# Kernel tuning notes

Measured on AMD Instinct MI355X. Metric: run time of the kernel, lower is better.

Reference implementation:

```python
import jax, jax.numpy as jnp
import numpy as np

TEMP = 5.0      # torch_kmeans SoftKMeans default temperature
N_ITERS = 25    # fixed iteration count (tolerance-based stop removed for jit)
EPS = 1e-9


def _soft_kmeans(x, l, key):
    # x: (r, q, d) -> labels (r, q) int32, centers (r, l, d)
    r, q, d = x.shape
    keys = jax.random.split(key, r)
    # random-point init (one permutation per batch, first l points)
    idx = jax.vmap(lambda k: jax.random.permutation(k, q)[:l])(keys)  # (r, l)
    centers = jnp.take_along_axis(x, idx[:, :, None], axis=1)         # (r, l, d)
    x_sq = jnp.sum(x * x, axis=-1)                                    # (r, q)

    def dist_to(centers):
        # squared euclidean distance (r, q, l)
        return (x_sq[:, :, None]
                - 2.0 * jnp.einsum('rqd,rld->rql', x, centers)
                + jnp.sum(centers * centers, axis=-1)[:, None, :])

    def step(centers, _):
        w = jax.nn.softmax(-TEMP * dist_to(centers), axis=-1)         # (r, q, l)
        denom = jnp.sum(w, axis=1)[:, :, None] + EPS                  # (r, l, 1)
        centers = jnp.einsum('rql,rqd->rld', w, x) / denom
        return centers, None

    centers, _ = jax.lax.scan(step, centers, None, length=N_ITERS)
    labels = jnp.argmin(dist_to(centers), axis=-1)                    # (r, q)
    return labels, centers


def setup_inputs() -> dict:
    key = jax.random.key(0)
    x = jax.random.normal(key, (8, 2048, 1024), dtype=jnp.float32)
    return {"x": x, "q": 4096, "r": 8, "l": 256}


def reference(x, q, r, l):
    B, T, F = x.shape
    # B*T*F must equal r*q*d; mirrors x.view(B,-1).view(B,q,-1).view(r,q,-1)
    xr = x.reshape(r, q, -1)
    labels, centers = _soft_kmeans(xr, l, jax.random.key(42))
    # gather centroid per point: rec[b, i, :] = centers[b, labels[b, i], :]
    rec = jnp.take_along_axis(centers, labels[:, :, None], axis=1)    # (r, q, d)
    return rec.reshape(B, T, F)
```

## Files before the change

### kernel.cpp

```cpp
#include <hip/hip_runtime.h>
#include <stdint.h>

#define RB 8
#define QN 4096
#define DN 512
#define LN 256
#define NITERS 25

__device__ __forceinline__ void tf2x32(uint32_t k0, uint32_t k1,
                                       uint32_t x0, uint32_t x1,
                                       uint32_t& y0, uint32_t& y1) {
  uint32_t ks2 = k0 ^ k1 ^ 0x1BD11BDAu;
#define TFR(r) { x0 += x1; x1 = (x1 << (r)) | (x1 >> (32 - (r))); x1 ^= x0; }
  x0 += k0; x1 += k1;
  TFR(13) TFR(15) TFR(26) TFR(6)   x0 += k1;  x1 += ks2 + 1u;
  TFR(17) TFR(29) TFR(16) TFR(24)  x0 += ks2; x1 += k0 + 2u;
  TFR(13) TFR(15) TFR(26) TFR(6)   x0 += k0;  x1 += k1 + 3u;
  TFR(17) TFR(29) TFR(16) TFR(24)  x0 += k1;  x1 += ks2 + 4u;
  TFR(13) TFR(15) TFR(26) TFR(6)   x0 += ks2; x1 += k0 + 5u;
#undef TFR
  y0 = x0; y1 = x1;
}

__global__ __launch_bounds__(1024) void k_init(const float* __restrict__ x,
                                               float* __restrict__ centers) {
  __shared__ unsigned long long comp[QN];
  __shared__ unsigned short perm[QN];
  __shared__ unsigned short ptmp[QN];
  const int b = blockIdx.x, t = threadIdx.x;

  uint32_t kb0, kb1;
  tf2x32(0u, 42u, 0u, (uint32_t)b, kb0, kb1);

  for (int i = t; i < QN; i += 1024) perm[i] = (unsigned short)i;
  __syncthreads();

  for (int round = 0; round < 2; ++round) {
    uint32_t nk0, nk1, sk0, sk1;
    tf2x32(kb0, kb1, 0u, 0u, nk0, nk1);
    tf2x32(kb0, kb1, 0u, 1u, sk0, sk1);
    kb0 = nk0; kb1 = nk1;
    for (int i = t; i < QN; i += 1024) {
      uint32_t y0, y1;
      tf2x32(sk0, sk1, 0u, (uint32_t)i, y0, y1);
      uint32_t bits = y0 ^ y1;
      comp[i] = ((unsigned long long)bits << 32) | (unsigned)i;
    }
    __syncthreads();
    for (int k = 2; k <= QN; k <<= 1) {
      for (int j = k >> 1; j > 0; j >>= 1) {
        for (int i = t; i < QN; i += 1024) {
          int ixj = i ^ j;
          if (ixj > i) {
            unsigned long long vi = comp[i], vj = comp[ixj];
            bool up = ((i & k) == 0);
            bool sw = up ? (vi > vj) : (vi < vj);
            if (sw) { comp[i] = vj; comp[ixj] = vi; }
          }
        }
        __syncthreads();
      }
    }
    for (int i = t; i < QN; i += 1024) ptmp[i] = perm[(unsigned)(comp[i] & 0xFFFFu)];
    __syncthreads();
    for (int i = t; i < QN; i += 1024) perm[i] = ptmp[i];
    __syncthreads();
  }

  const float4* xb = (const float4*)(x + (size_t)b * QN * DN);
  float4* cb = (float4*)(centers + (size_t)b * LN * DN);
  for (int e = t; e < LN * (DN / 4); e += 1024) {
    int row = e >> 7;
    int c = e & 127;
    cb[(size_t)row * 128 + c] = xb[(size_t)perm[row] * 128 + c];
  }
}

__global__ __launch_bounds__(256) void k_rowsq_d(const float* __restrict__ a,
                                                 double* __restrict__ o, int nrows) {
  int w = (blockIdx.x * 256 + threadIdx.x) >> 6;
  int lane = threadIdx.x & 63;
  if (w >= nrows) return;
  const float* row = a + (size_t)w * DN;
  double s = 0.0;
  for (int i = lane; i < DN; i += 64) { double v = (double)row[i]; s = fma(v, v, s); }
#pragma unroll
  for (int off = 32; off; off >>= 1) s += __shfl_down(s, off);
  if (lane == 0) o[w] = s;
}

#define QT 64
#define DK 16
#define XLD 82
#define CLDf 260
__device__ __forceinline__ int grow(int q) { return q + ((q >> 3) << 1); }

__global__ __launch_bounds__(256, 2) void k_assign(const float* __restrict__ x,
                                                   const float* __restrict__ centers,
                                                   const double* __restrict__ csqd,
                                                   float* __restrict__ W) {
  __shared__ double xsD[DK][XLD];
  __shared__ float  csF[DK][CLDf];
  __shared__ double red[QT][33];
  const int b = blockIdx.y, q0 = blockIdx.x * QT, t = threadIdx.x;
  const int rg = t & 7, cg = t >> 3;
  double acc[8][8];
#pragma unroll
  for (int i = 0; i < 8; i++)
#pragma unroll
    for (int j = 0; j < 8; j++) acc[i][j] = 0.0;

  const float* xb = x + ((size_t)b * QN + q0) * DN;
  const float* cb = centers + (size_t)b * LN * DN;
  const int xrow = t >> 2, xc4 = t & 3;
  const int xg = grow(xrow);

  float4 gx, gc[4];
  gx = *(const float4*)(xb + (size_t)xrow * DN + xc4 * 4);
#pragma unroll
  for (int i = 0; i < 4; i++) {
    int f = t + 256 * i; int row = f >> 2, c4 = f & 3;
    gc[i] = *(const float4*)(cb + (size_t)row * DN + c4 * 4);
  }

  for (int d0 = 0; d0 < DN; d0 += DK) {
    xsD[xc4 * 4 + 0][xg] = (double)gx.x; xsD[xc4 * 4 + 1][xg] = (double)gx.y;
    xsD[xc4 * 4 + 2][xg] = (double)gx.z; xsD[xc4 * 4 + 3][xg] = (double)gx.w;
#pragma unroll
    for (int i = 0; i < 4; i++) {
      int f = t + 256 * i; int row = f >> 2, c4 = f & 3;
      csF[c4 * 4 + 0][row] = gc[i].x; csF[c4 * 4 + 1][row] = gc[i].y;
      csF[c4 * 4 + 2][row] = gc[i].z; csF[c4 * 4 + 3][row] = gc[i].w;
    }
    __syncthreads();
    if (d0 + DK < DN) {
      gx = *(const float4*)(xb + (size_t)xrow * DN + (d0 + DK) + xc4 * 4);
#pragma unroll
      for (int i = 0; i < 4; i++) {
        int f = t + 256 * i; int row = f >> 2, c4 = f & 3;
        gc[i] = *(const float4*)(cb + (size_t)row * DN + (d0 + DK) + c4 * 4);
      }
    }
    double xva[8]; float4 ca0, ca1;
#pragma unroll
    for (int j = 0; j < 8; j++) xva[j] = xsD[0][rg * 10 + j];
    ca0 = *(const float4*)&csF[0][cg * 8];
    ca1 = *(const float4*)&csF[0][cg * 8 + 4];
#pragma unroll
    for (int k = 0; k < DK; k++) {
      double xvb[8]; float4 cb0, cb1;
      if (k + 1 < DK) {
#pragma unroll
        for (int j = 0; j < 8; j++) xvb[j] = xsD[k + 1][rg * 10 + j];
        cb0 = *(const float4*)&csF[k + 1][cg * 8];
        cb1 = *(const float4*)&csF[k + 1][cg * 8 + 4];
      }
      double cv[8] = {(double)ca0.x, (double)ca0.y, (double)ca0.z, (double)ca0.w,
                      (double)ca1.x, (double)ca1.y, (double)ca1.z, (double)ca1.w};
#pragma unroll
      for (int i = 0; i < 8; i++)
#pragma unroll
        for (int j = 0; j < 8; j++)
          acc[i][j] = fma(xva[i], cv[j], acc[i][j]);
      if (k + 1 < DK) {
#pragma unroll
        for (int j = 0; j < 8; j++) xva[j] = xvb[j];
        ca0 = cb0; ca1 = cb1;
      }
    }
    __syncthreads();
  }

  double csqv[8];
#pragma unroll
  for (int j = 0; j < 8; j++) csqv[j] = csqd[b * LN + cg * 8 + j];

  double lmax[8];
#pragma unroll
  for (int i = 0; i < 8; i++) {
    double m = -1e300;
#pragma unroll
    for (int j = 0; j < 8; j++) {
      double lg = -5.0 * (csqv[j] - 2.0 * acc[i][j]);
      acc[i][j] = lg;
      m = fmax(m, lg);
    }
    lmax[i] = m;
  }
#pragma unroll
  for (int i = 0; i < 8; i++) red[rg * 8 + i][cg] = lmax[i];
  __syncthreads();
  double rmax[8];
#pragma unroll
  for (int i = 0; i < 8; i++) {
    double m = -1e300;
    for (int c = 0; c < 32; c++) m = fmax(m, red[rg * 8 + i][c]);
    rmax[i] = m;
  }
  __syncthreads();
#pragma unroll
  for (int i = 0; i < 8; i++) {
    double s = 0.0;
#pragma unroll
    for (int j = 0; j < 8; j++) {
      double e = exp(acc[i][j] - rmax[i]);
      acc[i][j] = e;
      s += e;
    }
    red[rg * 8 + i][cg] = s;
  }
  __syncthreads();
#pragma unroll
  for (int i = 0; i < 8; i++) {
    double s = 0.0;
    for (int c = 0; c < 32; c++) s += red[rg * 8 + i][c];
    float* wrow = W + ((size_t)b * QN + q0 + rg * 8 + i) * LN + cg * 8;
    float4 v0 = make_float4((float)(acc[i][0] / s), (float)(acc[i][1] / s),
                            (float)(acc[i][2] / s), (float)(acc[i][3] / s));
    float4 v1 = make_float4((float)(acc[i][4] / s), (float)(acc[i][5] / s),
                            (float)(acc[i][6] / s), (float)(acc[i][7] / s));
    *(float4*)wrow = v0;
    *(float4*)(wrow + 4) = v1;
  }
}

#define NCH 8
#define CHQ (QN / NCH)
#define UKQ 16

__global__ __launch_bounds__(256, 2) void k_update_split(
    const float* __restrict__ W, const float* __restrict__ x,
    float* __restrict__ P, float* __restrict__ dsum) {
  __shared__ float wT[UKQ][132];
  __shared__ float xT[UKQ][132];
  const int b = blockIdx.z;
  const int s = blockIdx.y;
  const int lt = (blockIdx.x >> 2) * 128;
  const int dt = (blockIdx.x & 3) * 128;
  const int t = threadIdx.x;
  const int tr = t >> 4, tc = t & 15;
  float acc[8][8];
#pragma unroll
  for (int i = 0; i < 8; i++)
#pragma unroll
    for (int j = 0; j < 8; j++) acc[i][j] = 0.f;
  float dsm[8] = {0, 0, 0, 0, 0, 0, 0, 0};

  const float* Wb = W + ((size_t)b * QN + (size_t)s * CHQ) * LN + lt;
  const float* xb = x + ((size_t)b * QN + (size_t)s * CHQ) * DN + dt;

  float4 gw[2], gx2[2];
#pragma unroll
  for (int i = 0; i < 2; i++) {
    int f = t + 256 * i; int row = f >> 5, c = f & 31;
    gw[i]  = *(const float4*)(Wb + (size_t)row * LN + c * 4);
    gx2[i] = *(const float4*)(xb + (size_t)row * DN + c * 4);
  }

  for (int k0 = 0; k0 < CHQ; k0 += UKQ) {
#pragma unroll
    for (int i = 0; i < 2; i++) {
      int f = t + 256 * i; int row = f >> 5, c = f & 31;
      *(float4*)&wT[row][c * 4] = gw[i];
      *(float4*)&xT[row][c * 4] = gx2[i];
    }
    __syncthreads();
    if (k0 + UKQ < CHQ) {
#pragma unroll
      for (int i = 0; i < 2; i++) {
        int f = t + 256 * i; int row = f >> 5, c = f & 31;
        gw[i]  = *(const float4*)(Wb + (size_t)(k0 + UKQ + row) * LN + c * 4);
        gx2[i] = *(const float4*)(xb + (size_t)(k0 + UKQ + row) * DN + c * 4);
      }
    }
    float4 wa0, wa1, xa0, xa1;
    wa0 = *(const float4*)&wT[0][tr * 4];  wa1 = *(const float4*)&wT[0][64 + tr * 4];
    xa0 = *(const float4*)&xT[0][tc * 4];  xa1 = *(const float4*)&xT[0][64 + tc * 4];
#pragma unroll
    for (int k = 0; k < UKQ; k++) {
      float4 wb0, wb1, xb0, xb1;
      if (k + 1 < UKQ) {
        wb0 = *(const float4*)&wT[k + 1][tr * 4];  wb1 = *(const float4*)&wT[k + 1][64 + tr * 4];
        xb0 = *(const float4*)&xT[k + 1][tc * 4];  xb1 = *(const float4*)&xT[k + 1][64 + tc * 4];
      }
      float wf[8] = {wa0.x, wa0.y, wa0.z, wa0.w, wa1.x, wa1.y, wa1.z, wa1.w};
      float xf[8] = {xa0.x, xa0.y, xa0.z, xa0.w, xa1.x, xa1.y, xa1.z, xa1.w};
#pragma unroll
      for (int i = 0; i < 8; i++) {
        dsm[i] += wf[i];
#pragma unroll
        for (int j = 0; j < 8; j++) acc[i][j] = fmaf(wf[i], xf[j], acc[i][j]);
      }
      if (k + 1 < UKQ) { wa0 = wb0; wa1 = wb1; xa0 = xb0; xa1 = xb1; }
    }
    __syncthreads();
  }

#pragma unroll
  for (int i = 0; i < 8; i++) {
    int l = lt + ((i < 4) ? (tr * 4 + i) : (64 + tr * 4 + i - 4));
    float* prow = P + (((size_t)s * RB + b) * LN + l) * DN + dt;
    *(float4*)(prow + tc * 4)      = make_float4(acc[i][0], acc[i][1], acc[i][2], acc[i][3]);
    *(float4*)(prow + 64 + tc * 4) = make_float4(acc[i][4], acc[i][5], acc[i][6], acc[i][7]);
    if (tc == 0) dsum[((size_t)s * RB + b) * LN + l] = dsm[i];
  }
}

__global__ __launch_bounds__(128) void k_reduce(const float* __restrict__ P,
                                                const float* __restrict__ dsum,
                                                float* __restrict__ cnew,
                                                double* __restrict__ csqd) {
  const int row = blockIdx.x;
  const int b = row >> 8, l = row & 255;
  const int t = threadIdx.x;
  float dn = 0.f;
#pragma unroll
  for (int s = 0; s < NCH; s++) dn += dsum[((size_t)s * RB + b) * LN + l];
  float den = dn + 1e-9f;
  float4 v = make_float4(0.f, 0.f, 0.f, 0.f);
#pragma unroll
  for (int s = 0; s < NCH; s++) {
    float4 p = *(const float4*)(P + (((size_t)s * RB + b) * LN + l) * DN + t * 4);
    v.x += p.x; v.y += p.y; v.z += p.z; v.w += p.w;
  }
  float4 o = make_float4(v.x / den, v.y / den, v.z / den, v.w / den);
  *(float4*)(cnew + ((size_t)b * LN + l) * DN + t * 4) = o;
  double sq = (double)o.x * o.x + (double)o.y * o.y +
              (double)o.z * o.z + (double)o.w * o.w;
#pragma unroll
  for (int off = 32; off; off >>= 1) sq += __shfl_down(sq, off);
  __shared__ double sred[2];
  if ((t & 63) == 0) sred[t >> 6] = sq;
  __syncthreads();
  if (t == 0) csqd[row] = sred[0] + sred[1];
}

#define LT 64
#define DT 64
#define KQ 32
__global__ __launch_bounds__(256) void k_update_mono(const float* __restrict__ W,
                                                     const float* __restrict__ x,
                                                     float* __restrict__ cnew) {
  __shared__ float wT[KQ][LT + 4];
  __shared__ float xT[KQ][DT + 4];
  const int b = blockIdx.z;
  const int l0 = blockIdx.x * LT;
  const int d0 = blockIdx.y * DT;
  const int t = threadIdx.x;
  const int rg = t & 15;
  const int cg = t >> 4;
  float acc[4][4];
#pragma unroll
  for (int i = 0; i < 4; i++)
#pragma unroll
    for (int j = 0; j < 4; j++) acc[i][j] = 0.f;
  float dsm[4] = {0.f, 0.f, 0.f, 0.f};
  const float* Wb = W + (size_t)b * QN * LN;
  const float* xb = x + (size_t)b * QN * DN;
  for (int k0 = 0; k0 < QN; k0 += KQ) {
#pragma unroll
    for (int i = 0; i < 2; i++) {
      int f = t + 256 * i;
      int row = f >> 4, c4 = f & 15;
      *(float4*)&wT[row][c4 * 4] = *(const float4*)(Wb + (size_t)(k0 + row) * LN + l0 + c4 * 4);
    }
#pragma unroll
    for (int i = 0; i < 2; i++) {
      int f = t + 256 * i;
      int row = f >> 4, c4 = f & 15;
      *(float4*)&xT[row][c4 * 4] = *(const float4*)(xb + (size_t)(k0 + row) * DN + d0 + c4 * 4);
    }
    __syncthreads();
#pragma unroll
    for (int k = 0; k < KQ; k++) {
      float wf[4], xf[4];
      *(float4*)wf = *(const float4*)&wT[k][rg * 4];
      *(float4*)xf = *(const float4*)&xT[k][cg * 4];
#pragma unroll
      for (int i = 0; i < 4; i++) {
        dsm[i] += wf[i];
#pragma unroll
        for (int j = 0; j < 4; j++) acc[i][j] = fmaf(wf[i], xf[j], acc[i][j]);
      }
    }
    __syncthreads();
  }
#pragma unroll
  for (int i = 0; i < 4; i++) {
    float den = dsm[i] + 1e-9f;
    *(float4*)(cnew + ((size_t)b * LN + l0 + rg * 4 + i) * DN + d0 + cg * 4) =
        make_float4(acc[i][0] / den, acc[i][1] / den, acc[i][2] / den, acc[i][3] / den);
  }
}

__global__ __launch_bounds__(256, 2) void k_final(const float* __restrict__ x,
                                                  const float* __restrict__ centers,
                                                  const double* __restrict__ csqd,
                                                  float* __restrict__ out) {
  __shared__ double xsD[DK][XLD];
  __shared__ float  csF[DK][CLDf];
  __shared__ double redv[QT][33];
  __shared__ unsigned short redi[QT][33];
  __shared__ unsigned short labels[QT];
  const int b = blockIdx.y, q0 = blockIdx.x * QT, t = threadIdx.x;
  const int rg = t & 7, cg = t >> 3;
  double acc[8][8];
#pragma unroll
  for (int i = 0; i < 8; i++)
#pragma unroll
    for (int j = 0; j < 8; j++) acc[i][j] = 0.0;

  const float* xb = x + ((size_t)b * QN + q0) * DN;
  const float* cb = centers + (size_t)b * LN * DN;
  const int xrow = t >> 2, xc4 = t & 3;
  const int xg = grow(xrow);

  float4 gx, gc[4];
  gx = *(const float4*)(xb + (size_t)xrow * DN + xc4 * 4);
#pragma unroll
  for (int i = 0; i < 4; i++) {
    int f = t + 256 * i; int row = f >> 2, c4 = f & 3;
    gc[i] = *(const float4*)(cb + (size_t)row * DN + c4 * 4);
  }

  for (int d0 = 0; d0 < DN; d0 += DK) {
    xsD[xc4 * 4 + 0][xg] = (double)gx.x; xsD[xc4 * 4 + 1][xg] = (double)gx.y;
    xsD[xc4 * 4 + 2][xg] = (double)gx.z; xsD[xc4 * 4 + 3][xg] = (double)gx.w;
#pragma unroll
    for (int i = 0; i < 4; i++) {
      int f = t + 256 * i; int row = f >> 2, c4 = f & 3;
      csF[c4 * 4 + 0][row] = gc[i].x; csF[c4 * 4 + 1][row] = gc[i].y;
      csF[c4 * 4 + 2][row] = gc[i].z; csF[c4 * 4 + 3][row] = gc[i].w;
    }
    __syncthreads();
    if (d0 + DK < DN) {
      gx = *(const float4*)(xb + (size_t)xrow * DN + (d0 + DK) + xc4 * 4);
#pragma unroll
      for (int i = 0; i < 4; i++) {
        int f = t + 256 * i; int row = f >> 2, c4 = f & 3;
        gc[i] = *(const float4*)(cb + (size_t)row * DN + (d0 + DK) + c4 * 4);
      }
    }
    double xva[8]; float4 ca0, ca1;
#pragma unroll
    for (int j = 0; j < 8; j++) xva[j] = xsD[0][rg * 10 + j];
    ca0 = *(const float4*)&csF[0][cg * 8];
    ca1 = *(const float4*)&csF[0][cg * 8 + 4];
#pragma unroll
    for (int k = 0; k < DK; k++) {
      double xvb[8]; float4 cb0, cb1;
      if (k + 1 < DK) {
#pragma unroll
        for (int j = 0; j < 8; j++) xvb[j] = xsD[k + 1][rg * 10 + j];
        cb0 = *(const float4*)&csF[k + 1][cg * 8];
        cb1 = *(const float4*)&csF[k + 1][cg * 8 + 4];
      }
      double cv[8] = {(double)ca0.x, (double)ca0.y, (double)ca0.z, (double)ca0.w,
                      (double)ca1.x, (double)ca1.y, (double)ca1.z, (double)ca1.w};
#pragma unroll
      for (int i = 0; i < 8; i++)
#pragma unroll
        for (int j = 0; j < 8; j++)
          acc[i][j] = fma(xva[i], cv[j], acc[i][j]);
      if (k + 1 < DK) {
#pragma unroll
        for (int j = 0; j < 8; j++) xva[j] = xvb[j];
        ca0 = cb0; ca1 = cb1;
      }
    }
    __syncthreads();
  }

  double csqv[8];
#pragma unroll
  for (int j = 0; j < 8; j++) csqv[j] = csqd[b * LN + cg * 8 + j];

  double bv[8]; int bi[8];
#pragma unroll
  for (int i = 0; i < 8; i++) {
    bv[i] = 1e300; bi[i] = 0;
#pragma unroll
    for (int j = 0; j < 8; j++) {
      double dd = csqv[j] - 2.0 * acc[i][j];
      if (dd < bv[i]) { bv[i] = dd; bi[i] = cg * 8 + j; }
    }
  }
#pragma unroll
  for (int i = 0; i < 8; i++) {
    redv[rg * 8 + i][cg] = bv[i];
    redi[rg * 8 + i][cg] = (unsigned short)bi[i];
  }
  __syncthreads();
  if (t < QT) {
    double best = 1e300; int bidx = 0;
    for (int c = 0; c < 32; c++) {
      double v = redv[t][c];
      int id = redi[t][c];
      if (v < best || (v == best && id < bidx)) { best = v; bidx = id; }
    }
    labels[t] = (unsigned short)bidx;
  }
  __syncthreads();
  const float4* cb4 = (const float4*)(centers + (size_t)b * LN * DN);
  float4* ob = (float4*)(out + ((size_t)b * QN + q0) * DN);
  for (int e = t; e < QT * (DN / 4); e += 256) {
    int row = e >> 7, c = e & 127;
    ob[(size_t)row * 128 + c] = cb4[(size_t)labels[row] * 128 + c];
  }
}

extern "C" void kernel_launch(void* const* d_in, const int* in_sizes, int n_in,
                              void* d_out, int out_size, void* d_ws, size_t ws_size,
                              hipStream_t stream) {
  const float* x = (const float*)d_in[0];
  float* out = (float*)d_out;

  const size_t szC    = (size_t)RB * LN * DN * sizeof(float);
  const size_t szCsqD = (size_t)RB * LN * sizeof(double);
  const size_t szDsum = (size_t)NCH * RB * LN * sizeof(float);
  const size_t szW    = (size_t)RB * QN * LN * sizeof(float);

  char* p = (char*)d_ws;
  float*  cA   = (float*)p;  p += szC;
  float*  cB   = (float*)p;  p += szC;
  double* csqd = (double*)p; p += szCsqD;
  float*  dsum = (float*)p;  p += szDsum;
  const bool bigws = ws_size >= 2 * szC + szCsqD + szDsum + szW;
  float* W = bigws ? (float*)p : (float*)d_out;
  float* P = (float*)d_out;

  k_init<<<RB, 1024, 0, stream>>>(x, cA);
  k_rowsq_d<<<(RB * LN) / 4, 256, 0, stream>>>(cA, csqd, RB * LN);

  float* cur = cA;
  float* nxt = cB;
  for (int it = 0; it < NITERS; ++it) {
    k_assign<<<dim3(QN / QT, RB), 256, 0, stream>>>(x, cur, csqd, W);
    if (bigws) {
      k_update_split<<<dim3(8, NCH, RB), 256, 0, stream>>>(W, x, P, dsum);
      k_reduce<<<RB * LN, 128, 0, stream>>>(P, dsum, nxt, csqd);
    } else {
      k_update_mono<<<dim3(LN / LT, DN / DT, RB), 256, 0, stream>>>(W, x, nxt);
      k_rowsq_d<<<(RB * LN) / 4, 256, 0, stream>>>(nxt, csqd, RB * LN);
    }
    float* tmp = cur; cur = nxt; nxt = tmp;
  }
  k_final<<<dim3(QN / QT, RB), 256, 0, stream>>>(x, cur, csqd, out);
}
```

Baseline: 7.982 ms.

## Load distance-GEMM operands directly from global memory, drop LDS staging

The fp64 distance GEMM in k_assign and k_final no longer stages x and centers through shared memory with double-buffered register prefetch. Each thread now reads its own 8 x-rows and 8 center-rows straight from global memory in float4 chunks and relies on the caches for reuse. This removes the __syncthreads barriers and shared-memory traffic but puts many redundant global/L1 loads into the FP64 inner loop. Separately, k_update_split drops its manual register prefetch of the LDS tiles and raises its occupancy hint from 2 to 3 blocks per CU.

New measurement: 12.58 ms. 1.58x slower.

```diff
diff --git a/kernel.cpp b/kernel.cpp
--- a/kernel.cpp
+++ b/kernel.cpp
@@ -90,17 +90,11 @@
 }
 
 #define QT 64
-#define DK 16
-#define XLD 82
-#define CLDf 260
-__device__ __forceinline__ int grow(int q) { return q + ((q >> 3) << 1); }
 
 __global__ __launch_bounds__(256, 2) void k_assign(const float* __restrict__ x,
                                                    const float* __restrict__ centers,
                                                    const double* __restrict__ csqd,
                                                    float* __restrict__ W) {
-  __shared__ double xsD[DK][XLD];
-  __shared__ float  csF[DK][CLDf];
   __shared__ double red[QT][33];
   const int b = blockIdx.y, q0 = blockIdx.x * QT, t = threadIdx.x;
   const int rg = t & 7, cg = t >> 3;
@@ -110,65 +104,30 @@
 #pragma unroll
     for (int j = 0; j < 8; j++) acc[i][j] = 0.0;
 
-  const float* xb = x + ((size_t)b * QN + q0) * DN;
-  const float* cb = centers + (size_t)b * LN * DN;
-  const int xrow = t >> 2, xc4 = t & 3;
-  const int xg = grow(xrow);
-
-  float4 gx, gc[4];
-  gx = *(const float4*)(xb + (size_t)xrow * DN + xc4 * 4);
-#pragma unroll
-  for (int i = 0; i < 4; i++) {
-    int f = t + 256 * i; int row = f >> 2, c4 = f & 3;
-    gc[i] = *(const float4*)(cb + (size_t)row * DN + c4 * 4);
-  }
-
-  for (int d0 = 0; d0 < DN; d0 += DK) {
-    xsD[xc4 * 4 + 0][xg] = (double)gx.x; xsD[xc4 * 4 + 1][xg] = (double)gx.y;
-    xsD[xc4 * 4 + 2][xg] = (double)gx.z; xsD[xc4 * 4 + 3][xg] = (double)gx.w;
-#pragma unroll
-    for (int i = 0; i < 4; i++) {
-      int f = t + 256 * i; int row = f >> 2, c4 = f & 3;
-      csF[c4 * 4 + 0][row] = gc[i].x; csF[c4 * 4 + 1][row] = gc[i].y;
-      csF[c4 * 4 + 2][row] = gc[i].z; csF[c4 * 4 + 3][row] = gc[i].w;
-    }
-    __syncthreads();
-    if (d0 + DK < DN) {
-      gx = *(const float4*)(xb + (size_t)xrow * DN + (d0 + DK) + xc4 * 4);
-#pragma unroll
-      for (int i = 0; i < 4; i++) {
-        int f = t + 256 * i; int row = f >> 2, c4 = f & 3;
-        gc[i] = *(const float4*)(cb + (size_t)row * DN + (d0 + DK) + c4 * 4);
-      }
-    }
-    double xva[8]; float4 ca0, ca1;
-#pragma unroll
-    for (int j = 0; j < 8; j++) xva[j] = xsD[0][rg * 10 + j];
-    ca0 = *(const float4*)&csF[0][cg * 8];
-    ca1 = *(const float4*)&csF[0][cg * 8 + 4];
-#pragma unroll
-    for (int k = 0; k < DK; k++) {
-      double xvb[8]; float4 cb0, cb1;
-      if (k + 1 < DK) {
-#pragma unroll
-        for (int j = 0; j < 8; j++) xvb[j] = xsD[k + 1][rg * 10 + j];
-        cb0 = *(const float4*)&csF[k + 1][cg * 8];
-        cb1 = *(const float4*)&csF[k + 1][cg * 8 + 4];
-      }
-      double cv[8] = {(double)ca0.x, (double)ca0.y, (double)ca0.z, (double)ca0.w,
-                      (double)ca1.x, (double)ca1.y, (double)ca1.z, (double)ca1.w};
-#pragma unroll
-      for (int i = 0; i < 8; i++)
+  const float* xb = x + ((size_t)b * QN + q0 + rg * 8) * DN;
+  const float* cb = centers + ((size_t)b * LN + cg * 8) * DN;
+
+  for (int d0 = 0; d0 < DN; d0 += 4) {
+    float xf[8][4], cf[8][4];
+#pragma unroll
+    for (int i = 0; i < 8; i++)
+      *(float4*)xf[i] = *(const float4*)(xb + (size_t)i * DN + d0);
+#pragma unroll
+    for (int j = 0; j < 8; j++)
+      *(float4*)cf[j] = *(const float4*)(cb + (size_t)j * DN + d0);
+#pragma unroll
+    for (int k = 0; k < 4; k++) {
+      double cd[8];
+#pragma unroll
+      for (int j = 0; j < 8; j++) cd[j] = (double)cf[j][k];
+#pragma unroll
+      for (int i = 0; i < 8; i++) {
+        double xd = (double)xf[i][k];
 #pragma unroll
         for (int j = 0; j < 8; j++)
-          acc[i][j] = fma(xva[i], cv[j], acc[i][j]);
-      if (k + 1 < DK) {
-#pragma unroll
-        for (int j = 0; j < 8; j++) xva[j] = xvb[j];
-        ca0 = cb0; ca1 = cb1;
-      }
-    }
-    __syncthreads();
+          acc[i][j] = fma(xd, cd[j], acc[i][j]);
+      }
+    }
   }
 
   double csqv[8];
@@ -228,7 +187,7 @@
 #define CHQ (QN / NCH)
 #define UKQ 16
 
-__global__ __launch_bounds__(256, 2) void k_update_split(
+__global__ __launch_bounds__(256, 3) void k_update_split(
     const float* __restrict__ W, const float* __restrict__ x,
     float* __restrict__ P, float* __restrict__ dsum) {
   __shared__ float wT[UKQ][132];
@@ -273,25 +232,20 @@
         gx2[i] = *(const float4*)(xb + (size_t)(k0 + UKQ + row) * DN + c * 4);
       }
     }
-    float4 wa0, wa1, xa0, xa1;
-    wa0 = *(const float4*)&wT[0][tr * 4];  wa1 = *(const float4*)&wT[0][64 + tr * 4];
-    xa0 = *(const float4*)&xT[0][tc * 4];  xa1 = *(const float4*)&xT[0][64 + tc * 4];
 #pragma unroll
     for (int k = 0; k < UKQ; k++) {
-      float4 wb0, wb1, xb0, xb1;
-      if (k + 1 < UKQ) {
-        wb0 = *(const float4*)&wT[k + 1][tr * 4];  wb1 = *(const float4*)&wT[k + 1][64 + tr * 4];
-        xb0 = *(const float4*)&xT[k + 1][tc * 4];  xb1 = *(const float4*)&xT[k + 1][64 + tc * 4];
-      }
-      float wf[8] = {wa0.x, wa0.y, wa0.z, wa0.w, wa1.x, wa1.y, wa1.z, wa1.w};
-      float xf[8] = {xa0.x, xa0.y, xa0.z, xa0.w, xa1.x, xa1.y, xa1.z, xa1.w};
+      float4 w0 = *(const float4*)&wT[k][tr * 4];
+      float4 w1 = *(const float4*)&wT[k][64 + tr * 4];
+      float4 x0 = *(const float4*)&xT[k][tc * 4];
+      float4 x1 = *(const float4*)&xT[k][64 + tc * 4];
+      float wf[8] = {w0.x, w0.y, w0.z, w0.w, w1.x, w1.y, w1.z, w1.w};
+      float xf[8] = {x0.x, x0.y, x0.z, x0.w, x1.x, x1.y, x1.z, x1.w};
 #pragma unroll
       for (int i = 0; i < 8; i++) {
         dsm[i] += wf[i];
 #pragma unroll
         for (int j = 0; j < 8; j++) acc[i][j] = fmaf(wf[i], xf[j], acc[i][j]);
       }
-      if (k + 1 < UKQ) { wa0 = wb0; wa1 = wb1; xa0 = xb0; xa1 = xb1; }
     }
     __syncthreads();
   }
@@ -397,8 +351,6 @@
                                                   const float* __restrict__ centers,
                                                   const double* __restrict__ csqd,
                                                   float* __restrict__ out) {
-  __shared__ double xsD[DK][XLD];
-  __shared__ float  csF[DK][CLDf];
   __shared__ double redv[QT][33];
   __shared__ unsigned short redi[QT][33];
   __shared__ unsigned short labels[QT];
@@ -410,65 +362,30 @@
 #pragma unroll
     for (int j = 0; j < 8; j++) acc[i][j] = 0.0;
 
-  const float* xb = x + ((size_t)b * QN + q0) * DN;
-  const float* cb = centers + (size_t)b * LN * DN;
-  const int xrow = t >> 2, xc4 = t & 3;
-  const int xg = grow(xrow);
-
-  float4 gx, gc[4];
-  gx = *(const float4*)(xb + (size_t)xrow * DN + xc4 * 4);
-#pragma unroll
-  for (int i = 0; i < 4; i++) {
-    int f = t + 256 * i; int row = f >> 2, c4 = f & 3;
-    gc[i] = *(const float4*)(cb + (size_t)row * DN + c4 * 4);
-  }
-
-  for (int d0 = 0; d0 < DN; d0 += DK) {
-    xsD[xc4 * 4 + 0][xg] = (double)gx.x; xsD[xc4 * 4 + 1][xg] = (double)gx.y;
-    xsD[xc4 * 4 + 2][xg] = (double)gx.z; xsD[xc4 * 4 + 3][xg] = (double)gx.w;
-#pragma unroll
-    for (int i = 0; i < 4; i++) {
-      int f = t + 256 * i; int row = f >> 2, c4 = f & 3;
-      csF[c4 * 4 + 0][row] = gc[i].x; csF[c4 * 4 + 1][row] = gc[i].y;
-      csF[c4 * 4 + 2][row] = gc[i].z; csF[c4 * 4 + 3][row] = gc[i].w;
-    }
-    __syncthreads();
-    if (d0 + DK < DN) {
-      gx = *(const float4*)(xb + (size_t)xrow * DN + (d0 + DK) + xc4 * 4);
-#pragma unroll
-      for (int i = 0; i < 4; i++) {
-        int f = t + 256 * i; int row = f >> 2, c4 = f & 3;
-        gc[i] = *(const float4*)(cb + (size_t)row * DN + (d0 + DK) + c4 * 4);
-      }
-    }
-    double xva[8]; float4 ca0, ca1;
-#pragma unroll
-    for (int j = 0; j < 8; j++) xva[j] = xsD[0][rg * 10 + j];
-    ca0 = *(const float4*)&csF[0][cg * 8];
-    ca1 = *(const float4*)&csF[0][cg * 8 + 4];
-#pragma unroll
-    for (int k = 0; k < DK; k++) {
-      double xvb[8]; float4 cb0, cb1;
-      if (k + 1 < DK) {
-#pragma unroll
-        for (int j = 0; j < 8; j++) xvb[j] = xsD[k + 1][rg * 10 + j];
-        cb0 = *(const float4*)&csF[k + 1][cg * 8];
-        cb1 = *(const float4*)&csF[k + 1][cg * 8 + 4];
-      }
-      double cv[8] = {(double)ca0.x, (double)ca0.y, (double)ca0.z, (double)ca0.w,
-                      (double)ca1.x, (double)ca1.y, (double)ca1.z, (double)ca1.w};
-#pragma unroll
-      for (int i = 0; i < 8; i++)
+  const float* xb = x + ((size_t)b * QN + q0 + rg * 8) * DN;
+  const float* cb = centers + ((size_t)b * LN + cg * 8) * DN;
+
+  for (int d0 = 0; d0 < DN; d0 += 4) {
+    float xf[8][4], cf[8][4];
+#pragma unroll
+    for (int i = 0; i < 8; i++)
+      *(float4*)xf[i] = *(const float4*)(xb + (size_t)i * DN + d0);
+#pragma unroll
+    for (int j = 0; j < 8; j++)
+      *(float4*)cf[j] = *(const float4*)(cb + (size_t)j * DN + d0);
+#pragma unroll
+    for (int k = 0; k < 4; k++) {
+      double cd[8];
+#pragma unroll
+      for (int j = 0; j < 8; j++) cd[j] = (double)cf[j][k];
+#pragma unroll
+      for (int i = 0; i < 8; i++) {
+        double xd = (double)xf[i][k];
 #pragma unroll
         for (int j = 0; j < 8; j++)
-          acc[i][j] = fma(xva[i], cv[j], acc[i][j]);
-      if (k + 1 < DK) {
-#pragma unroll
-        for (int j = 0; j < 8; j++) xva[j] = xvb[j];
-        ca0 = cb0; ca1 = cb1;
-      }
-    }
-    __syncthreads();
+          acc[i][j] = fma(xd, cd[j], acc[i][j]);
+      }
+    }
   }
 
   double csqv[8];
```

## Compute assignment distances with FP64 MFMA, guarded by a runtime probe

Applied to the files above, without the earlier changes.

Adds an FP64 MFMA (16x16x4) version of the assignment kernel, which computes the x·centers dot products in double on matrix cores and fuses softmax through wave shuffles. A one-block probe kernel checks the MFMA operand layout against a scalar reference and sets a flag. Both assign kernels are launched each iteration, and the one the flag does not select exits at once, so a bad layout falls back to the original VALU path. The update kernel also drops its manual shared-memory register prefetch and raises its occupancy hint to 3 blocks. The cost is one extra near-empty kernel launch per iteration.

Result: slower. 8.289 ms (+3.8%).

```diff
diff --git a/kernel.cpp b/kernel.cpp
--- a/kernel.cpp
+++ b/kernel.cpp
@@ -6,6 +6,8 @@
 #define DN 512
 #define LN 256
 #define NITERS 25
+
+typedef double f64x4 __attribute__((ext_vector_type(4)));
 
 __device__ __forceinline__ void tf2x32(uint32_t k0, uint32_t k1,
                                        uint32_t x0, uint32_t x1,
@@ -89,16 +91,151 @@
   if (lane == 0) o[w] = s;
 }
 
+__global__ __launch_bounds__(64) void k_probe(int* __restrict__ flag) {
+  __shared__ double xT[16][17];
+  __shared__ double cT[16][17];
+  const int t = threadIdx.x;
+  for (int i = t; i < 256; i += 64) {
+    int r = i >> 4, d = i & 15;
+    xT[d][r] = (double)(r * 5 + d * 3 + 1);
+    cT[d][r] = (double)(r * 2 + d * 7 + 2);
+  }
+  __syncthreads();
+  const int kg = t >> 4, li = t & 15;
+  f64x4 acc = {0.0, 0.0, 0.0, 0.0};
+#pragma unroll
+  for (int kk = 0; kk < 4; kk++) {
+    double a  = xT[kk * 4 + kg][li];
+    double bv = cT[kk * 4 + kg][li];
+    acc = __builtin_amdgcn_mfma_f64_16x16x4f64(a, bv, acc, 0, 0, 0);
+  }
+  bool ok = true;
+#pragma unroll
+  for (int d = 0; d < 4; d++) {
+    int q = kg * 4 + d;
+    double ref = 0.0;
+    for (int dd = 0; dd < 16; dd++) ref += xT[dd][q] * cT[dd][li];
+    ok = ok && (acc[d] == ref);
+  }
+  unsigned long long vote = __ballot(ok);
+  if (t == 0) *flag = (vote == ~0ull) ? 1 : 0;
+}
+
 #define QT 64
+#define XPD 68
+#define CPD 260
+
+__global__ __launch_bounds__(256, 2) void k_assign_mfma(const float* __restrict__ x,
+                                                        const float* __restrict__ centers,
+                                                        const double* __restrict__ csqd,
+                                                        float* __restrict__ W,
+                                                        const int* __restrict__ flag) {
+  if (*flag == 0) return;
+  __shared__ double xT[16][XPD];
+  __shared__ double cT[16][CPD];
+  const int b = blockIdx.y, q0 = blockIdx.x * QT, t = threadIdx.x;
+  const int w = t >> 6, lane = t & 63;
+  const int kg = lane >> 4, li = lane & 15;
+
+  f64x4 acc[16];
+#pragma unroll
+  for (int i = 0; i < 16; i++) acc[i] = (f64x4){0.0, 0.0, 0.0, 0.0};
+
+  const float* xb = x + ((size_t)b * QN + q0) * DN;
+  const float* cb = centers + (size_t)b * LN * DN;
+  const int xrow = t >> 2, xc4 = t & 3;
+
+  float4 gx, gc[4];
+  gx = *(const float4*)(xb + (size_t)xrow * DN + xc4 * 4);
+#pragma unroll
+  for (int i = 0; i < 4; i++) {
+    int f = t + 256 * i; int row = f >> 2, c4 = f & 3;
+    gc[i] = *(const float4*)(cb + (size_t)row * DN + c4 * 4);
+  }
+
+  for (int d0 = 0; d0 < DN; d0 += 16) {
+    xT[xc4 * 4 + 0][xrow] = (double)gx.x;
+    xT[xc4 * 4 + 1][xrow] = (double)gx.y;
+    xT[xc4 * 4 + 2][xrow] = (double)gx.z;
+    xT[xc4 * 4 + 3][xrow] = (double)gx.w;
+#pragma unroll
+    for (int i = 0; i < 4; i++) {
+      int f = t + 256 * i; int row = f >> 2, c4 = f & 3;
+      cT[c4 * 4 + 0][row] = (double)gc[i].x;
+      cT[c4 * 4 + 1][row] = (double)gc[i].y;
+      cT[c4 * 4 + 2][row] = (double)gc[i].z;
+      cT[c4 * 4 + 3][row] = (double)gc[i].w;
+    }
+    __syncthreads();
+    if (d0 + 16 < DN) {
+      gx = *(const float4*)(xb + (size_t)xrow * DN + (d0 + 16) + xc4 * 4);
+#pragma unroll
+      for (int i = 0; i < 4; i++) {
+        int f = t + 256 * i; int row = f >> 2, c4 = f & 3;
+        gc[i] = *(const float4*)(cb + (size_t)row * DN + (d0 + 16) + c4 * 4);
+      }
+    }
+#pragma unroll
+    for (int kk = 0; kk < 4; kk++) {
+      double a = xT[kk * 4 + kg][w * 16 + li];
+#pragma unroll
+      for (int t16 = 0; t16 < 16; t16++) {
+        double bv = cT[kk * 4 + kg][t16 * 16 + li];
+        acc[t16] = __builtin_amdgcn_mfma_f64_16x16x4f64(a, bv, acc[t16], 0, 0, 0);
+      }
+    }
+    __syncthreads();
+  }
+
+  double m[4] = {-1e300, -1e300, -1e300, -1e300};
+#pragma unroll
+  for (int t16 = 0; t16 < 16; t16++) {
+    double cq = csqd[b * LN + t16 * 16 + li];
+#pragma unroll
+    for (int d = 0; d < 4; d++) {
+      double lg = -5.0 * (cq - 2.0 * acc[t16][d]);
+      acc[t16][d] = lg;
+      m[d] = fmax(m[d], lg);
+    }
+  }
+#pragma unroll
+  for (int off = 1; off < 16; off <<= 1)
+#pragma unroll
+    for (int d = 0; d < 4; d++) m[d] = fmax(m[d], __shfl_xor(m[d], off, 64));
+
+  double s[4] = {0.0, 0.0, 0.0, 0.0};
+#pragma unroll
+  for (int t16 = 0; t16 < 16; t16++)
+#pragma unroll
+    for (int d = 0; d < 4; d++) {
+      double e = exp(acc[t16][d] - m[d]);
+      acc[t16][d] = e;
+      s[d] += e;
+    }
+#pragma unroll
+  for (int off = 1; off < 16; off <<= 1)
+#pragma unroll
+    for (int d = 0; d < 4; d++) s[d] += __shfl_xor(s[d], off, 64);
+
+  float* wbase = W + ((size_t)b * QN + q0 + w * 16 + kg * 4) * LN + li;
+#pragma unroll
+  for (int t16 = 0; t16 < 16; t16++)
+#pragma unroll
+    for (int d = 0; d < 4; d++)
+      wbase[(size_t)d * LN + t16 * 16] = (float)(acc[t16][d] / s[d]);
+}
+
 #define DK 16
 #define XLD 82
 #define CLDf 260
 __device__ __forceinline__ int grow(int q) { return q + ((q >> 3) << 1); }
 
-__global__ __launch_bounds__(256, 2) void k_assign(const float* __restrict__ x,
-                                                   const float* __restrict__ centers,
-                                                   const double* __restrict__ csqd,
-                                                   float* __restrict__ W) {
+__global__ __launch_bounds__(256, 2) void k_assign_valu(const float* __restrict__ x,
+                                                        const float* __restrict__ centers,
+                                                        const double* __restrict__ csqd,
+                                                        float* __restrict__ W,
+                                                        const int* __restrict__ flag) {
+  if (*flag != 0) return;
   __shared__ double xsD[DK][XLD];
   __shared__ float  csF[DK][CLDf];
   __shared__ double red[QT][33];
@@ -228,7 +365,7 @@
 #define CHQ (QN / NCH)
 #define UKQ 16
 
-__global__ __launch_bounds__(256, 2) void k_update_split(
+__global__ __launch_bounds__(256, 3) void k_update_split(
     const float* __restrict__ W, const float* __restrict__ x,
     float* __restrict__ P, float* __restrict__ dsum) {
   __shared__ float wT[UKQ][132];
@@ -273,25 +410,20 @@
         gx2[i] = *(const float4*)(xb + (size_t)(k0 + UKQ + row) * DN + c * 4);
       }
     }
-    float4 wa0, wa1, xa0, xa1;
-    wa0 = *(const float4*)&wT[0][tr * 4];  wa1 = *(const float4*)&wT[0][64 + tr * 4];
-    xa0 = *(const float4*)&xT[0][tc * 4];  xa1 = *(const float4*)&xT[0][64 + tc * 4];
 #pragma unroll
     for (int k = 0; k < UKQ; k++) {
-      float4 wb0, wb1, xb0, xb1;
-      if (k + 1 < UKQ) {
-        wb0 = *(const float4*)&wT[k + 1][tr * 4];  wb1 = *(const float4*)&wT[k + 1][64 + tr * 4];
-        xb0 = *(const float4*)&xT[k + 1][tc * 4];  xb1 = *(const float4*)&xT[k + 1][64 + tc * 4];
-      }
-      float wf[8] = {wa0.x, wa0.y, wa0.z, wa0.w, wa1.x, wa1.y, wa1.z, wa1.w};
-      float xf[8] = {xa0.x, xa0.y, xa0.z, xa0.w, xa1.x, xa1.y, xa1.z, xa1.w};
+      float4 w0 = *(const float4*)&wT[k][tr * 4];
+      float4 w1 = *(const float4*)&wT[k][64 + tr * 4];
+      float4 x0 = *(const float4*)&xT[k][tc * 4];
+      float4 x1 = *(const float4*)&xT[k][64 + tc * 4];
+      float wf[8] = {w0.x, w0.y, w0.z, w0.w, w1.x, w1.y, w1.z, w1.w};
+      float xf[8] = {x0.x, x0.y, x0.z, x0.w, x1.x, x1.y, x1.z, x1.w};
 #pragma unroll
       for (int i = 0; i < 8; i++) {
         dsm[i] += wf[i];
 #pragma unroll
         for (int j = 0; j < 8; j++) acc[i][j] = fmaf(wf[i], xf[j], acc[i][j]);
       }
-      if (k + 1 < UKQ) { wa0 = wb0; wa1 = wb1; xa0 = xb0; xa1 = xb1; }
     }
     __syncthreads();
   }
@@ -518,6 +650,7 @@
   const size_t szC    = (size_t)RB * LN * DN * sizeof(float);
   const size_t szCsqD = (size_t)RB * LN * sizeof(double);
   const size_t szDsum = (size_t)NCH * RB * LN * sizeof(float);
+  const size_t szFlag = 256;
   const size_t szW    = (size_t)RB * QN * LN * sizeof(float);
 
   char* p = (char*)d_ws;
@@ -525,17 +658,20 @@
   float*  cB   = (float*)p;  p += szC;
   double* csqd = (double*)p; p += szCsqD;
   float*  dsum = (float*)p;  p += szDsum;
-  const bool bigws = ws_size >= 2 * szC + szCsqD + szDsum + szW;
+  int*    flag = (int*)p;    p += szFlag;
+  const bool bigws = ws_size >= 2 * szC + szCsqD + szDsum + szFlag + szW;
   float* W = bigws ? (float*)p : (float*)d_out;
   float* P = (float*)d_out;
 
+  k_probe<<<1, 64, 0, stream>>>(flag);
   k_init<<<RB, 1024, 0, stream>>>(x, cA);
   k_rowsq_d<<<(RB * LN) / 4, 256, 0, stream>>>(cA, csqd, RB * LN);
 
   float* cur = cA;
   float* nxt = cB;
   for (int it = 0; it < NITERS; ++it) {
-    k_assign<<<dim3(QN / QT, RB), 256, 0, stream>>>(x, cur, csqd, W);
+    k_assign_mfma<<<dim3(QN / QT, RB), 256, 0, stream>>>(x, cur, csqd, W, flag);
+    k_assign_valu<<<dim3(QN / QT, RB), 256, 0, stream>>>(x, cur, csqd, W, flag);
     if (bigws) {
       k_update_split<<<dim3(8, NCH, RB), 256, 0, stream>>>(W, x, P, dsum);
       k_reduce<<<RB * LN, 128, 0, stream>>>(P, dsum, nxt, csqd);
```
